# Performance work log

Hardware: AMD Instinct MI355X
Metric: run time of the kernel (lower is better)

## Reference

```python
import jax, jax.numpy as jnp
import numpy as np

B, IN, H = 8192, 1024, 1024


def setup_inputs() -> dict:
    key = jax.random.key(0)
    ks = jax.random.split(key, 6)
    s = 1.0 / np.sqrt(H)
    return {
        "incoming": jax.random.normal(ks[0], (B, IN), dtype=jnp.float32),
        "state": jax.random.normal(ks[1], (2, B, H), dtype=jnp.float32),
        "Wx": jax.random.normal(ks[2], (4 * H, IN), dtype=jnp.float32) * s,
        "bx": jax.random.normal(ks[3], (4 * H,), dtype=jnp.float32) * s,
        "Wh": jax.random.normal(ks[4], (4 * H, H), dtype=jnp.float32) * s,
        "bh": jax.random.normal(ks[5], (4 * H,), dtype=jnp.float32) * s,
    }


def reference(incoming, state, Wx, bx, Wh, bh):
    # Fused form of 8 Linear layers: gates stacked in (i, f, g, o) order.
    h_prev, c_prev = state[0], state[1]
    gates = (jnp.einsum('bi,gi->bg', incoming, Wx) + bx
             + jnp.einsum('bh,gh->bg', h_prev, Wh) + bh)  # [B, 4H]
    i_g, f_g, g_g, o_g = jnp.split(gates, 4, axis=-1)
    i = jax.nn.sigmoid(i_g)
    f = jax.nn.sigmoid(f_g)
    g = jnp.tanh(g_g)
    o = jax.nn.sigmoid(o_g)
    new_c = f * c_prev + i * g
    new_h = o * jnp.tanh(new_c)
    # output == new_h; return stacked (new_h, new_c) as [2, B, H]
    return jnp.stack([new_h, new_c])
```

## Files before the change

kernel.cpp:

```cpp
#include <hip/hip_runtime.h>
#include <hip/hip_bf16.h>


#define B_DIM 8192
#define H_DIM 1024
#define BH (8192 * 1024)
#define K2 2048

typedef __attribute__((ext_vector_type(4))) float f32x4;
typedef __attribute__((ext_vector_type(8))) __bf16 bf16x8;
typedef __attribute__((ext_vector_type(8))) unsigned short ushort8;

static __device__ __forceinline__ unsigned short f2bf(float f) {
    return __builtin_bit_cast(unsigned short, (__bf16)f);
}
static __device__ __forceinline__ float sigf(float x) {
    return 1.0f / (1.0f + __expf(-x));
}
static __device__ __forceinline__ float tanhft(float x) {
    float e = __expf(2.0f * x);
    return (e - 1.0f) / (e + 1.0f);
}
static __device__ __forceinline__ void gload16(const void* g, void* l) {
    __builtin_amdgcn_global_load_lds(
        (const __attribute__((address_space(1))) unsigned int*)g,
        (__attribute__((address_space(3))) unsigned int*)l, 16, 0, 0);
}
static __device__ __forceinline__ ushort8 cvt8(const float* src) {
    const float4 u = ((const float4*)src)[0];
    const float4 v = ((const float4*)src)[1];
    ushort8 o;
    o[0] = f2bf(u.x); o[1] = f2bf(u.y); o[2] = f2bf(u.z); o[3] = f2bf(u.w);
    o[4] = f2bf(v.x); o[5] = f2bf(v.y); o[6] = f2bf(v.z); o[7] = f2bf(v.w);
    return o;
}

__global__ __launch_bounds__(256) void conv_kernel(
    const float* __restrict__ x, const float* __restrict__ h,
    const float* __restrict__ Wx, const float* __restrict__ Wh,
    unsigned short* __restrict__ A, unsigned short* __restrict__ W)
{
    const int bidx = blockIdx.x;
    if (bidx < 8192) {
        const int id = bidx * 256 + threadIdx.x;
        const int base = id * 8;
        const int b = base >> 11;
        const int k = base & 2047;
        const float* src = (k < 1024) ? (x + (size_t)b * 1024 + k)
                                      : (h + (size_t)b * 1024 + (k - 1024));
        *(ushort8*)(A + base) = cvt8(src);
    } else {
        const int id = (bidx - 8192) * 256 + threadIdx.x;
        const int base = id * 8;
        const int n = base >> 11;
        const int k = base & 2047;
        const int jb = n >> 8, wn = (n >> 6) & 3, g = (n >> 4) & 3, jj = n & 15;
        const int srow = (g << 10) + (jb << 6) + (wn << 4) + jj;
        const float* src = (k < 1024) ? (Wx + (size_t)srow * 1024 + k)
                                      : (Wh + (size_t)srow * 1024 + (k - 1024));
        *(ushort8*)(W + base) = cvt8(src);
    }
}

__global__ __launch_bounds__(512, 2) void lstm_gemm8(
    const unsigned short* __restrict__ Abf, const unsigned short* __restrict__ Wbf,
    const float* __restrict__ bx, const float* __restrict__ bh,
    const float* __restrict__ cprev, float* __restrict__ out)
{
    extern __shared__ unsigned short lds[];

    const int tid = threadIdx.x;
    const int lane = tid & 63;
    const int wv = tid >> 6;
    const int wm = wv >> 2;
    const int wn = wv & 3;
    const int q = lane >> 4, c = lane & 15;

    const int bid = blockIdx.x;
    const int xcd = bid & 7;
    const int idx = bid >> 3;
    const int jb  = xcd * 2 + (idx & 1);
    const int bb  = idx >> 1;
    const int b0 = bb * 256;

    const unsigned short* Ab = Abf + (size_t)b0 * K2;
    const unsigned short* Wb = Wbf + (size_t)(jb * 256) * K2;

    const int srow = tid >> 2;
    const int sk8g = (tid & 3) ^ ((tid >> 3) & 3);
    const size_t ss0 = (size_t)srow * K2 + (size_t)sk8g * 8;
    const unsigned sdst = (unsigned)(tid & 448) * 8;

    const int cq = ((q ^ ((c >> 1) & 3)) << 3);
    const unsigned aoff = (unsigned)(wm * 128 + c) * 32 + cq;
    const unsigned boff = 16384u + (unsigned)(wn * 64 + c) * 32 + cq;

    f32x4 acc[8][4];
#pragma unroll
    for (int m = 0; m < 8; ++m)
#pragma unroll
        for (int g = 0; g < 4; ++g) acc[m][g] = f32x4{0.f, 0.f, 0.f, 0.f};

    bf16x8 av[4], bv[4];

#define STAGE(TP, T, ISB, KS) do {                                             \
    const unsigned short* _s = (ISB) ? Wb : Ab;                                \
    const size_t _o = ss0 + (size_t)((T) & 31) * 64 + (KS) * 32;               \
    const unsigned _d = ((TP) << 15) | ((ISB) << 14) | ((KS) << 13);           \
    gload16(_s + _o, &lds[_d + sdst]);                                         \
    gload16(_s + (size_t)128 * K2 + _o, &lds[_d + 4096u + sdst]);              \
} while (0)

#define LOADA(BUF, KS, MH) do {                                                \
    const unsigned short* _p = lds + (BUF) * 32768 + (KS) * 8192 + aoff + (MH) * 2048; \
    av[0] = *(const bf16x8*)(_p);                                              \
    av[1] = *(const bf16x8*)(_p + 512);                                        \
    av[2] = *(const bf16x8*)(_p + 1024);                                       \
    av[3] = *(const bf16x8*)(_p + 1536);                                       \
} while (0)

#define LOADB(BUF, KS) do {                                                    \
    const unsigned short* _p = lds + (BUF) * 32768 + (KS) * 8192 + boff;       \
    bv[0] = *(const bf16x8*)(_p);                                              \
    bv[1] = *(const bf16x8*)(_p + 512);                                        \
    bv[2] = *(const bf16x8*)(_p + 1024);                                       \
    bv[3] = *(const bf16x8*)(_p + 1536);                                       \
} while (0)

#define MFMA16(MH) do {                                                        \
    __builtin_amdgcn_s_setprio(1);                                             \
    _Pragma("unroll")                                                          \
    for (int _i = 0; _i < 4; ++_i)                                             \
        _Pragma("unroll")                                                      \
        for (int _g = 0; _g < 4; ++_g)                                         \
            acc[(MH) * 4 + _i][_g] = __builtin_amdgcn_mfma_f32_16x16x32_bf16(  \
                av[_i], bv[_g], acc[(MH) * 4 + _i][_g], 0, 0, 0);              \
    __builtin_amdgcn_s_setprio(0);                                             \
} while (0)

#define BAR()    __builtin_amdgcn_s_barrier()
#define WLGKM0() asm volatile("s_waitcnt lgkmcnt(0)")
#define WVM4()   asm volatile("s_waitcnt vmcnt(4)" ::: "memory")

#define PH(BUF, KS, MH, RB, STP, ST, SB, SK) do {                              \
    LOADA(BUF, KS, MH);                                                        \
    if (RB) LOADB(BUF, KS);                                                    \
    STAGE(STP, ST, SB, SK);                                                    \
    BAR();                                                                     \
    WLGKM0();                                                                  \
    MFMA16(MH);                                                                \
    BAR();                                                                     \
} while (0)

#define PHV(BUF, KS, MH, STP, ST, SB, SK) do {                                 \
    LOADA(BUF, KS, MH);                                                        \
    STAGE(STP, ST, SB, SK);                                                    \
    BAR();                                                                     \
    WLGKM0();                                                                  \
    MFMA16(MH);                                                                \
    WVM4();                                                                    \
    BAR();                                                                     \
} while (0)

    STAGE(0, 0, 0, 0); STAGE(0, 0, 1, 0); STAGE(0, 0, 0, 1); STAGE(0, 0, 1, 1);
    STAGE(1, 1, 0, 0); STAGE(1, 1, 1, 0);
    WVM4();
    BAR();

    for (int u = 0; u < 32; u += 2) {
        PH (0, 0, 0, 1, 1, u + 1, 0, 1);
        PH (0, 0, 1, 0, 1, u + 1, 1, 1);
        PH (0, 1, 0, 1, 0, u + 2, 0, 0);
        PHV(0, 1, 1,    0, u + 2, 1, 0);
        PH (1, 0, 0, 1, 0, u + 2, 0, 1);
        PH (1, 0, 1, 0, 0, u + 2, 1, 1);
        PH (1, 1, 0, 1, 1, u + 3, 0, 0);
        PHV(1, 1, 1,    1, u + 3, 1, 0);
    }

#undef PH
#undef PHV
#undef STAGE
#undef LOADA
#undef LOADB
#undef MFMA16

    const int j = jb * 64 + wn * 16 + c;
    const float bI = bx[j] + bh[j];
    const float bF = bx[1024 + j] + bh[1024 + j];
    const float bG = bx[2048 + j] + bh[2048 + j];
    const float bO = bx[3072 + j] + bh[3072 + j];
#pragma unroll
    for (int mt = 0; mt < 8; ++mt) {
#pragma unroll
        for (int rr = 0; rr < 4; ++rr) {
            const int row = b0 + wm * 128 + mt * 16 + q * 4 + rr;
            const size_t off = (size_t)row * 1024 + j;
            const float iv = sigf(acc[mt][0][rr] + bI);
            const float fv = sigf(acc[mt][1][rr] + bF);
            const float gv = tanhft(acc[mt][2][rr] + bG);
            const float ov = sigf(acc[mt][3][rr] + bO);
            const float cp = cprev[off];
            const float nc = fv * cp + iv * gv;
            out[off] = ov * tanhft(nc);
            out[BH + off] = nc;
        }
    }
}

__global__ __launch_bounds__(256) void lstm_fallback(
    const float* __restrict__ incoming, const float* __restrict__ state,
    const float* __restrict__ Wx, const float* __restrict__ bx,
    const float* __restrict__ Wh, const float* __restrict__ bh,
    float* __restrict__ out)
{
    __shared__ unsigned short lA[128 * 64];
    __shared__ unsigned short lW[128 * 64];
    const int t = threadIdx.x;
    const int lane = t & 63;
    const int wv = t >> 6;
    const int q = lane >> 4;
    const int c = lane & 15;
    const int j0 = blockIdx.x * 32;
    const int b0 = blockIdx.y * 128;
    const float* hprev = state;
    const float* cprev = state + (size_t)BH;

    f32x4 acc[2][8];
#pragma unroll
    for (int mt = 0; mt < 2; ++mt)
#pragma unroll
        for (int nt = 0; nt < 8; ++nt)
            acc[mt][nt] = f32x4{0.f, 0.f, 0.f, 0.f};

    const int sr = t >> 3;
    const int sk8 = t & 7;

    for (int it = 0; it < 32; ++it) {
        const bool first = (it < 16);
        const float* As = first ? incoming : hprev;
        const float* Ws = first ? Wx : Wh;
        const int kk = first ? it * 64 : it * 64 - 1024;
#pragma unroll
        for (int i = 0; i < 4; ++i) {
            const int r = i * 32 + sr;
            *(ushort8*)&lA[r * 64 + ((sk8 ^ (r & 7)) * 8)] =
                cvt8(As + (size_t)(b0 + r) * 1024 + kk + sk8 * 8);
        }
#pragma unroll
        for (int i = 0; i < 4; ++i) {
            const int n = i * 32 + sr;
            const int grow = ((n >> 5) << 10) + j0 + (n & 31);
            *(ushort8*)&lW[n * 64 + ((sk8 ^ (n & 7)) * 8)] =
                cvt8(Ws + (size_t)grow * 1024 + kk + sk8 * 8);
        }
        __syncthreads();
#pragma unroll
        for (int ks = 0; ks < 2; ++ks) {
            const int k8a = ks * 4 + q;
            bf16x8 av[2], bv[8];
#pragma unroll
            for (int mt = 0; mt < 2; ++mt) {
                const int r = wv * 32 + mt * 16 + c;
                av[mt] = *(const bf16x8*)&lA[r * 64 + ((k8a ^ (r & 7)) * 8)];
            }
#pragma unroll
            for (int nt = 0; nt < 8; ++nt) {
                const int n = nt * 16 + c;
                bv[nt] = *(const bf16x8*)&lW[n * 64 + ((k8a ^ (n & 7)) * 8)];
            }
#pragma unroll
            for (int mt = 0; mt < 2; ++mt)
#pragma unroll
                for (int nt = 0; nt < 8; ++nt)
                    acc[mt][nt] = __builtin_amdgcn_mfma_f32_16x16x32_bf16(
                        av[mt], bv[nt], acc[mt][nt], 0, 0, 0);
        }
        __syncthreads();
    }

    const int b0r = b0 + wv * 32;
#pragma unroll
    for (int jt = 0; jt < 2; ++jt) {
        const int j = j0 + jt * 16 + c;
        const float bI = bx[j] + bh[j];
        const float bF = bx[1024 + j] + bh[1024 + j];
        const float bG = bx[2048 + j] + bh[2048 + j];
        const float bO = bx[3072 + j] + bh[3072 + j];
#pragma unroll
        for (int mt = 0; mt < 2; ++mt) {
#pragma unroll
            for (int rr = 0; rr < 4; ++rr) {
                const int row = b0r + mt * 16 + q * 4 + rr;
                const size_t off = (size_t)row * 1024 + j;
                const float iv = sigf(acc[mt][0 + jt][rr] + bI);
                const float fv = sigf(acc[mt][2 + jt][rr] + bF);
                const float gv = tanhft(acc[mt][4 + jt][rr] + bG);
                const float ov = sigf(acc[mt][6 + jt][rr] + bO);
                const float cp = cprev[off];
                const float nc = fv * cp + iv * gv;
                out[off] = ov * tanhft(nc);
                out[BH + off] = nc;
            }
        }
    }
}

extern "C" void kernel_launch(void* const* d_in, const int* in_sizes, int n_in,
                              void* d_out, int out_size, void* d_ws, size_t ws_size,
                              hipStream_t stream) {
    const float* incoming = (const float*)d_in[0];
    const float* state    = (const float*)d_in[1];
    const float* Wx       = (const float*)d_in[2];
    const float* bx       = (const float*)d_in[3];
    const float* Wh       = (const float*)d_in[4];
    const float* bh       = (const float*)d_in[5];
    float* out = (float*)d_out;

    const float* hprev = state;
    const float* cprev = state + (size_t)BH;

    const size_t A_bytes = (size_t)B_DIM * K2 * 2;
    const size_t W_bytes = (size_t)4 * H_DIM * K2 * 2;

    if (ws_size >= A_bytes + W_bytes) {
        unsigned short* Abf = (unsigned short*)d_ws;
        unsigned short* Wbf = (unsigned short*)((char*)d_ws + A_bytes);
        conv_kernel<<<dim3(12288), dim3(256), 0, stream>>>(
            incoming, hprev, Wx, Wh, Abf, Wbf);
        (void)hipFuncSetAttribute((const void*)lstm_gemm8,
                                  hipFuncAttributeMaxDynamicSharedMemorySize, 131072);
        lstm_gemm8<<<dim3(512), dim3(512), 131072, stream>>>(
            Abf, Wbf, bx, bh, cprev, out);
    } else {
        dim3 grid(H_DIM / 32, B_DIM / 128);
        lstm_fallback<<<grid, dim3(256), 0, stream>>>(
            incoming, state, Wx, bx, Wh, bh, out);
    }
}
```

Baseline: 166.8 us.

## Restage LDS as full 64-wide k-tiles with XOR swizzle and retimed loads

```diff
diff --git a/kernel.cpp b/kernel.cpp
--- a/kernel.cpp
+++ b/kernel.cpp
@@ -86,14 +86,13 @@
     const unsigned short* Ab = Abf + (size_t)b0 * K2;
     const unsigned short* Wb = Wbf + (size_t)(jb * 256) * K2;
 
-    const int srow = tid >> 2;
-    const int sk8g = (tid & 3) ^ ((tid >> 3) & 3);
-    const size_t ss0 = (size_t)srow * K2 + (size_t)sk8g * 8;
-    const unsigned sdst = (unsigned)(tid & 448) * 8;
-
-    const int cq = ((q ^ ((c >> 1) & 3)) << 3);
-    const unsigned aoff = (unsigned)(wm * 128 + c) * 32 + cq;
-    const unsigned boff = 16384u + (unsigned)(wn * 64 + c) * 32 + cq;
+    const size_t ssg = (size_t)(tid >> 3) * K2
+                     + (size_t)(((tid & 7) ^ ((tid >> 3) & 7)) * 8);
+    const unsigned sbase = (unsigned)(tid & 448) * 8;
+
+    const unsigned arow = (unsigned)(wm * 128 + c) * 64;
+    const unsigned brow = 16384u + (unsigned)(wn * 64 + c) * 64;
+    const unsigned cach = (unsigned)((q ^ (c & 7)) << 3);
 
     f32x4 acc[8][4];
 #pragma unroll
@@ -103,28 +102,28 @@
 
     bf16x8 av[4], bv[4];
 
-#define STAGE(TP, T, ISB, KS) do {                                             \
+#define STG(BUF, ISB, QA, T) do {                                              \
     const unsigned short* _s = (ISB) ? Wb : Ab;                                \
-    const size_t _o = ss0 + (size_t)((T) & 31) * 64 + (KS) * 32;               \
-    const unsigned _d = ((TP) << 15) | ((ISB) << 14) | ((KS) << 13);           \
-    gload16(_s + _o, &lds[_d + sdst]);                                         \
-    gload16(_s + (size_t)128 * K2 + _o, &lds[_d + 4096u + sdst]);              \
+    gload16(_s + ssg + (size_t)(QA) * 64 * K2 + (size_t)((T) & 31) * 64,       \
+            &lds[(BUF) * 32768 + (ISB) * 16384 + (QA) * 4096 + sbase]);        \
 } while (0)
 
 #define LOADA(BUF, KS, MH) do {                                                \
-    const unsigned short* _p = lds + (BUF) * 32768 + (KS) * 8192 + aoff + (MH) * 2048; \
+    const unsigned short* _p = lds + (BUF) * 32768 + (MH) * 4096 + arow        \
+                             + (cach ^ ((KS) * 32));                           \
     av[0] = *(const bf16x8*)(_p);                                              \
-    av[1] = *(const bf16x8*)(_p + 512);                                        \
-    av[2] = *(const bf16x8*)(_p + 1024);                                       \
-    av[3] = *(const bf16x8*)(_p + 1536);                                       \
+    av[1] = *(const bf16x8*)(_p + 1024);                                       \
+    av[2] = *(const bf16x8*)(_p + 2048);                                       \
+    av[3] = *(const bf16x8*)(_p + 3072);                                       \
 } while (0)
 
 #define LOADB(BUF, KS) do {                                                    \
-    const unsigned short* _p = lds + (BUF) * 32768 + (KS) * 8192 + boff;       \
+    const unsigned short* _p = lds + (BUF) * 32768 + brow                      \
+                             + (cach ^ ((KS) * 32));                           \
     bv[0] = *(const bf16x8*)(_p);                                              \
-    bv[1] = *(const bf16x8*)(_p + 512);                                        \
-    bv[2] = *(const bf16x8*)(_p + 1024);                                       \
-    bv[3] = *(const bf16x8*)(_p + 1536);                                       \
+    bv[1] = *(const bf16x8*)(_p + 1024);                                       \
+    bv[2] = *(const bf16x8*)(_p + 2048);                                       \
+    bv[3] = *(const bf16x8*)(_p + 3072);                                       \
 } while (0)
 
 #define MFMA16(MH) do {                                                        \
@@ -140,47 +139,35 @@
 
 #define BAR()    __builtin_amdgcn_s_barrier()
 #define WLGKM0() asm volatile("s_waitcnt lgkmcnt(0)")
-#define WVM4()   asm volatile("s_waitcnt vmcnt(4)" ::: "memory")
-
-#define PH(BUF, KS, MH, RB, STP, ST, SB, SK) do {                              \
-    LOADA(BUF, KS, MH);                                                        \
-    if (RB) LOADB(BUF, KS);                                                    \
-    STAGE(STP, ST, SB, SK);                                                    \
-    BAR();                                                                     \
-    WLGKM0();                                                                  \
-    MFMA16(MH);                                                                \
-    BAR();                                                                     \
-} while (0)
-
-#define PHV(BUF, KS, MH, STP, ST, SB, SK) do {                                 \
-    LOADA(BUF, KS, MH);                                                        \
-    STAGE(STP, ST, SB, SK);                                                    \
-    BAR();                                                                     \
-    WLGKM0();                                                                  \
-    MFMA16(MH);                                                                \
-    WVM4();                                                                    \
-    BAR();                                                                     \
-} while (0)
-
-    STAGE(0, 0, 0, 0); STAGE(0, 0, 1, 0); STAGE(0, 0, 0, 1); STAGE(0, 0, 1, 1);
-    STAGE(1, 1, 0, 0); STAGE(1, 1, 1, 0);
-    WVM4();
+#define WVM2()   asm volatile("s_waitcnt vmcnt(2)" ::: "memory")
+
+#define TILE(BUF, T1) do {                                                     \
+    LOADA(BUF, 0, 0); LOADB(BUF, 0);                                           \
+    STG((BUF) ^ 1, 1, 0, T1); STG((BUF) ^ 1, 1, 1, T1);                        \
+    BAR(); WLGKM0(); MFMA16(0); WVM2(); BAR();                                 \
+    LOADA(BUF, 0, 1);                                                          \
+    STG((BUF) ^ 1, 1, 2, T1); STG((BUF) ^ 1, 1, 3, T1);                        \
+    BAR(); WLGKM0(); MFMA16(1); BAR();                                         \
+    LOADA(BUF, 1, 0); LOADB(BUF, 1);                                           \
+    STG((BUF) ^ 1, 0, 0, T1); STG((BUF) ^ 1, 0, 2, T1);                        \
+    BAR(); WLGKM0(); MFMA16(0); BAR();                                         \
+    LOADA(BUF, 1, 1);                                                          \
+    STG((BUF) ^ 1, 0, 1, T1); STG((BUF) ^ 1, 0, 3, T1);                        \
+    BAR(); WLGKM0(); MFMA16(1); WVM2(); BAR();                                 \
+} while (0)
+
+    STG(0, 1, 0, 0); STG(0, 1, 1, 0); STG(0, 1, 2, 0); STG(0, 1, 3, 0);
+    STG(0, 0, 0, 0); STG(0, 0, 2, 0); STG(0, 0, 1, 0); STG(0, 0, 3, 0);
+    WVM2();
     BAR();
 
     for (int u = 0; u < 32; u += 2) {
-        PH (0, 0, 0, 1, 1, u + 1, 0, 1);
-        PH (0, 0, 1, 0, 1, u + 1, 1, 1);
-        PH (0, 1, 0, 1, 0, u + 2, 0, 0);
-        PHV(0, 1, 1,    0, u + 2, 1, 0);
-        PH (1, 0, 0, 1, 0, u + 2, 0, 1);
-        PH (1, 0, 1, 0, 0, u + 2, 1, 1);
-        PH (1, 1, 0, 1, 1, u + 3, 0, 0);
-        PHV(1, 1, 1,    1, u + 3, 1, 0);
-    }
-
-#undef PH
-#undef PHV
-#undef STAGE
+        TILE(0, u + 1);
+        TILE(1, u + 2);
+    }
+
+#undef TILE
+#undef STG
 #undef LOADA
 #undef LOADB
 #undef MFMA16
```

Result: faster. 159.2 us, median of 2 (-4.6%).
